# Kernel tuning notes

Measured on AMD Instinct MI355X. Metric: run time of the kernel, lower is better.

The kernel has to match this reference:

```python
import jax, jax.numpy as jnp
import numpy as np

D = 2048      # in_features == out_features == rank (forced by the module's shape algebra)
N = 8192
ALPHA = 16
SCALING = ALPHA / D
EPS = 1e-12   # F.normalize eps


def setup_inputs() -> dict:
    key = jax.random.key(0)
    kx, ka, kb, kd = jax.random.split(key, 4)
    x = jax.random.normal(kx, (N, D), dtype=jnp.float32)
    # Parameters per DoRALayer.__init__. Note: the original inits lora_B to zeros,
    # which makes the whole forward identically zero; we use small randn instead
    # so the baseline exercises non-trivial numerics (same math).
    lora_A = jax.random.normal(ka, (D, D), dtype=jnp.float32) * 0.01  # [rank, in]
    lora_B = jax.random.normal(kb, (D, D), dtype=jnp.float32) * 0.01  # [out, rank]
    magnitude = jnp.ones((D,), dtype=jnp.float32)                      # [out]
    direction = jax.random.normal(kd, (D, D), dtype=jnp.float32) * 0.01  # [out, rank]
    return {"x": x, "lora_A": lora_A, "lora_B": lora_B,
            "magnitude": magnitude, "direction": direction}


def reference(x, lora_A, lora_B, magnitude, direction):
    # W = lora_A.T @ lora_B.T  -> [in, out]
    W = jnp.einsum('ri,or->io', lora_A, lora_B)
    # F.linear(x, W) = x @ W.T  -> [N, in]
    lora_output = jnp.einsum('no,io->ni', x, W) * SCALING
    # torch.norm(magnitude): scalar L2 norm of the magnitude vector
    mag = jnp.linalg.norm(magnitude)
    # F.normalize(direction, p=2, dim=1) with eps clamp
    dnorm = jnp.sqrt(jnp.sum(direction * direction, axis=1, keepdims=True))
    dirn = direction / jnp.maximum(dnorm, EPS)
    # (direction @ lora_output.T).T  -> [N, out]
    dora_output = mag * jnp.einsum('or,nr->no', dirn, lora_output)
    return dora_output
```

## Files before the change

### kernel.cpp

```cpp
#include <hip/hip_runtime.h>

typedef unsigned short u16;
typedef unsigned int   u32;
typedef __attribute__((ext_vector_type(8))) __bf16 bf16x8;
typedef __attribute__((ext_vector_type(4))) float  f32x4;

#define D_DIM 2048
#define N_TOK 8192

__device__ __forceinline__ u16 f2bf(float f) {
  u32 u = __float_as_uint(f);
  u32 r = (u + 0x7fffu + ((u >> 16) & 1u)) >> 16;
  return (u16)r;
}

__device__ __forceinline__ void gl16(const void* g, void* l) {
  __builtin_amdgcn_global_load_lds((const __attribute__((address_space(1))) void*)g,
                                   (__attribute__((address_space(3))) void*)l,
                                   16, 0, 0);
}

__global__ __launch_bounds__(256) void cvt_f32_bf16(const float* __restrict__ in,
                                                    u16* __restrict__ out, int n4) {
  int idx = blockIdx.x * 256 + threadIdx.x;
  int stride = gridDim.x * 256;
  for (int i = idx; i < n4; i += stride) {
    float4 v = ((const float4*)in)[i];
    ushort4 o;
    o.x = f2bf(v.x); o.y = f2bf(v.y); o.z = f2bf(v.z); o.w = f2bf(v.w);
    ((ushort4*)out)[i] = o;
  }
}

__global__ __launch_bounds__(256) void normalize_rows(const float* __restrict__ dir,
                                                      u16* __restrict__ out) {
  const int row = blockIdx.x;
  const int tid = threadIdx.x;
  const float4* r = (const float4*)(dir + (size_t)row * D_DIM);
  float4 v0 = r[tid * 2 + 0];
  float4 v1 = r[tid * 2 + 1];
  float ss = v0.x*v0.x + v0.y*v0.y + v0.z*v0.z + v0.w*v0.w
           + v1.x*v1.x + v1.y*v1.y + v1.z*v1.z + v1.w*v1.w;
  #pragma unroll
  for (int off = 32; off > 0; off >>= 1) ss += __shfl_down(ss, off);
  __shared__ float red[4];
  __shared__ float invs;
  if ((tid & 63) == 0) red[tid >> 6] = ss;
  __syncthreads();
  if (tid == 0) {
    float t = red[0] + red[1] + red[2] + red[3];
    invs = 1.0f / fmaxf(sqrtf(t), 1e-12f);
  }
  __syncthreads();
  float inv = invs;
  ushort4 o0, o1;
  o0.x = f2bf(v0.x * inv); o0.y = f2bf(v0.y * inv);
  o0.z = f2bf(v0.z * inv); o0.w = f2bf(v0.w * inv);
  o1.x = f2bf(v1.x * inv); o1.y = f2bf(v1.y * inv);
  o1.z = f2bf(v1.z * inv); o1.w = f2bf(v1.w * inv);
  ushort4* ow = (ushort4*)(out + (size_t)row * D_DIM);
  ow[tid * 2 + 0] = o0;
  ow[tid * 2 + 1] = o1;
}

__global__ __launch_bounds__(256) void mag_scale_k(const float* __restrict__ m,
                                                   float* __restrict__ scale,
                                                   int n, float scaling) {
  const int tid = threadIdx.x;
  float ss = 0.0f;
  for (int i = tid; i < n / 4; i += 256) {
    float4 v = ((const float4*)m)[i];
    ss += v.x*v.x + v.y*v.y + v.z*v.z + v.w*v.w;
  }
  #pragma unroll
  for (int off = 32; off > 0; off >>= 1) ss += __shfl_down(ss, off);
  __shared__ float red[4];
  if ((tid & 63) == 0) red[tid >> 6] = ss;
  __syncthreads();
  if (tid == 0) {
    float t = red[0] + red[1] + red[2] + red[3];
    scale[0] = sqrtf(t) * scaling;
  }
}

template <int OUT_BF16>
__global__ __launch_bounds__(256)
void gemm_nt(const u16* __restrict__ A, const u16* __restrict__ B,
             void* __restrict__ Cv, int M, int Nn, int K,
             const float* __restrict__ scale_ptr) {
  __shared__ __align__(16) u16 lA[128 * 64];
  __shared__ __align__(16) u16 lB[128 * 64];
  const int tid  = threadIdx.x;
  const int lane = tid & 63;
  const int wave = tid >> 6;
  const int wr = wave >> 1, wc = wave & 1;
  const int row0 = blockIdx.y * 128, col0 = blockIdx.x * 128;

  const u16* Ag = A + (size_t)row0 * K;
  const u16* Bg = B + (size_t)col0 * K;

  f32x4 acc[4][4];
  #pragma unroll
  for (int i = 0; i < 4; ++i)
    #pragma unroll
    for (int j = 0; j < 4; ++j)
      acc[i][j] = (f32x4){0.0f, 0.0f, 0.0f, 0.0f};

  const int rsub = lane >> 3;
  const int sm   = lane & 7;

  for (int k0 = 0; k0 < K; k0 += 64) {
    #pragma unroll
    for (int j = 0; j < 4; ++j) {
      int c  = wave * 4 + j;
      int rt = c * 8 + rsub;
      int ssrc = sm ^ (rt & 7);
      gl16(Ag + (size_t)rt * K + k0 + ssrc * 8, &lA[c * 512 + lane * 8]);
      gl16(Bg + (size_t)rt * K + k0 + ssrc * 8, &lB[c * 512 + lane * 8]);
    }
    __syncthreads();

    #pragma unroll
    for (int ks = 0; ks < 2; ++ks) {
      bf16x8 af[4], bfr[4];
      #pragma unroll
      for (int mi = 0; mi < 4; ++mi) {
        int ra = wr * 64 + mi * 16 + (lane & 15);
        int sa = (ks * 4 + (lane >> 4)) ^ (ra & 7);
        af[mi] = *(const bf16x8*)&lA[ra * 64 + sa * 8];
        int rb = wc * 64 + mi * 16 + (lane & 15);
        int sb = (ks * 4 + (lane >> 4)) ^ (rb & 7);
        bfr[mi] = *(const bf16x8*)&lB[rb * 64 + sb * 8];
      }
      #pragma unroll
      for (int mi = 0; mi < 4; ++mi)
        #pragma unroll
        for (int ni = 0; ni < 4; ++ni)
          acc[mi][ni] = __builtin_amdgcn_mfma_f32_16x16x32_bf16(
              af[mi], bfr[ni], acc[mi][ni], 0, 0, 0);
    }
    __syncthreads();
  }

  float scl = scale_ptr ? scale_ptr[0] : 1.0f;
  const int orow = row0 + wr * 64 + (lane >> 4) * 4;
  const int ocol = col0 + wc * 64 + (lane & 15);
  #pragma unroll
  for (int mi = 0; mi < 4; ++mi) {
    #pragma unroll
    for (int ni = 0; ni < 4; ++ni) {
      #pragma unroll
      for (int r = 0; r < 4; ++r) {
        int gr = orow + mi * 16 + r;
        int gc = ocol + ni * 16;
        float v = acc[mi][ni][r] * scl;
        if (OUT_BF16) ((u16*)Cv)[(size_t)gr * Nn + gc] = f2bf(v);
        else          ((float*)Cv)[(size_t)gr * Nn + gc] = v;
      }
    }
  }
}

extern "C" void kernel_launch(void* const* d_in, const int* in_sizes, int n_in,
                              void* d_out, int out_size, void* d_ws, size_t ws_size,
                              hipStream_t stream) {
  const float* x    = (const float*)d_in[0];
  const float* lorA = (const float*)d_in[1];
  const float* lorB = (const float*)d_in[2];
  const float* mag  = (const float*)d_in[3];
  const float* dir  = (const float*)d_in[4];
  float* out = (float*)d_out;

  char* ws = (char*)d_ws;
  u16*   xb  = (u16*)(ws);
  u16*   Ab  = (u16*)(ws + 33554432);
  u16*   Bb  = (u16*)(ws + 41943040);
  u16*   Db  = (u16*)(ws + 50331648);
  u16*   CT  = (u16*)(ws + 58720256);
  float* scl = (float*)(ws + 67108864);
  u16*   WfT = Db;

  cvt_f32_bf16<<<2048, 256, 0, stream>>>(x,    xb, N_TOK * D_DIM / 4);
  cvt_f32_bf16<<<1024, 256, 0, stream>>>(lorA, Ab, D_DIM * D_DIM / 4);
  cvt_f32_bf16<<<1024, 256, 0, stream>>>(lorB, Bb, D_DIM * D_DIM / 4);
  normalize_rows<<<D_DIM, 256, 0, stream>>>(dir, Db);
  mag_scale_k<<<1, 256, 0, stream>>>(mag, scl, D_DIM, 16.0f / 2048.0f);

  gemm_nt<1><<<dim3(D_DIM / 128, D_DIM / 128), 256, 0, stream>>>(
      Db, Ab, CT, D_DIM, D_DIM, D_DIM, nullptr);
  gemm_nt<1><<<dim3(D_DIM / 128, D_DIM / 128), 256, 0, stream>>>(
      CT, Bb, WfT, D_DIM, D_DIM, D_DIM, nullptr);
  gemm_nt<0><<<dim3(D_DIM / 128, N_TOK / 128), 256, 0, stream>>>(
      xb, WfT, out, N_TOK, D_DIM, D_DIM, scl);
}
```

Baseline: 332.3 us.

## Use 256x256 double-buffered 8-wave GEMM for the large token projection

Result: faster. 312.9 us (-5.8%).

```diff
diff --git a/kernel.cpp b/kernel.cpp
--- a/kernel.cpp
+++ b/kernel.cpp
@@ -161,6 +161,138 @@
   }
 }
 
+#define STG(tile, half) do {                                                   \
+    const u16* G_ = ((half) < 2) ? (A + (size_t)(row0 + ((half)&1)*128) * K)   \
+                                 : (B + (size_t)(col0 + ((half)&1)*128) * K);  \
+    u16* L_ = &lds[(tile)&1][half][0];                                         \
+    const int k0_ = (tile) << 6;                                               \
+    { int idx = tid;       int rt = idx >> 3, sm2 = idx & 7;                   \
+      gl16(G_ + (size_t)rt*K + k0_ + (sm2 ^ (rt&7))*8, L_ + idx*8); }          \
+    { int idx = 512 + tid; int rt = idx >> 3, sm2 = idx & 7;                   \
+      gl16(G_ + (size_t)rt*K + k0_ + (sm2 ^ (rt&7))*8, L_ + idx*8); }          \
+  } while (0)
+
+#define RDA(b, mi, ks) (*(const bf16x8*)&lds[b][wr][((mi)*16 + fr)*64 + ((((ks)*4 + fs) ^ (fr & 7)))*8])
+#define RDB(b, ni, ks) (*(const bf16x8*)&lds[b][2 + ((wc*64 + (ni)*16 + fr) >> 7)][((wc*64 + (ni)*16 + fr) & 127)*64 + ((((ks)*4 + fs) ^ (fr & 7)))*8])
+#define MFMA(a, bb, c) __builtin_amdgcn_mfma_f32_16x16x32_bf16(a, bb, c, 0, 0, 0)
+
+template <int OUT_BF16>
+__global__ __launch_bounds__(512, 2)
+void gemm_nt8(const u16* __restrict__ A, const u16* __restrict__ B,
+              void* __restrict__ Cv, int M, int Nn, int K,
+              const float* __restrict__ scale_ptr) {
+  __shared__ __align__(16) u16 lds[2][4][128 * 64];
+  const int tid  = threadIdx.x;
+  const int lane = tid & 63;
+  const int wave = tid >> 6;
+  const int wr = wave >> 2;
+  const int wc = wave & 3;
+  const int row0 = blockIdx.y * 256, col0 = blockIdx.x * 256;
+  const int NT = K >> 6;
+  const int fr = lane & 15, fs = lane >> 4;
+
+  f32x4 acc[8][4];
+  #pragma unroll
+  for (int i = 0; i < 8; ++i)
+    #pragma unroll
+    for (int j = 0; j < 4; ++j)
+      acc[i][j] = (f32x4){0.0f, 0.0f, 0.0f, 0.0f};
+
+  STG(0, 0); STG(0, 1); STG(0, 2); STG(0, 3);
+  if (NT > 1) {
+    STG(1, 0); STG(1, 1); STG(1, 2); STG(1, 3);
+    asm volatile("s_waitcnt vmcnt(8)" ::: "memory");
+  } else {
+    asm volatile("s_waitcnt vmcnt(0)" ::: "memory");
+  }
+  __builtin_amdgcn_s_barrier();
+
+  for (int t = 0; t < NT; ++t) {
+    const int b = t & 1;
+    bf16x8 aF[8], bL[4], bH[4];
+
+    #pragma unroll
+    for (int mi = 0; mi < 4; ++mi) { aF[mi*2] = RDA(b, mi, 0); aF[mi*2+1] = RDA(b, mi, 1); }
+    #pragma unroll
+    for (int ni = 0; ni < 2; ++ni) { bL[ni*2] = RDB(b, ni, 0); bL[ni*2+1] = RDB(b, ni, 1); }
+    __builtin_amdgcn_s_barrier();
+    asm volatile("s_waitcnt lgkmcnt(0)");
+    __builtin_amdgcn_s_setprio(1);
+    #pragma unroll
+    for (int mi = 0; mi < 4; ++mi)
+      #pragma unroll
+      for (int ni = 0; ni < 2; ++ni)
+        #pragma unroll
+        for (int ks = 0; ks < 2; ++ks)
+          acc[mi][ni] = MFMA(aF[mi*2+ks], bL[ni*2+ks], acc[mi][ni]);
+    __builtin_amdgcn_s_setprio(0);
+    __builtin_amdgcn_s_barrier();
+
+    #pragma unroll
+    for (int ni = 0; ni < 2; ++ni) { bH[ni*2] = RDB(b, ni + 2, 0); bH[ni*2+1] = RDB(b, ni + 2, 1); }
+    __builtin_amdgcn_s_barrier();
+    asm volatile("s_waitcnt lgkmcnt(0)");
+    __builtin_amdgcn_s_setprio(1);
+    #pragma unroll
+    for (int mi = 0; mi < 4; ++mi)
+      #pragma unroll
+      for (int ni = 0; ni < 2; ++ni)
+        #pragma unroll
+        for (int ks = 0; ks < 2; ++ks)
+          acc[mi][ni + 2] = MFMA(aF[mi*2+ks], bH[ni*2+ks], acc[mi][ni + 2]);
+    __builtin_amdgcn_s_setprio(0);
+    __builtin_amdgcn_s_barrier();
+
+    #pragma unroll
+    for (int mi = 0; mi < 4; ++mi) { aF[mi*2] = RDA(b, mi + 4, 0); aF[mi*2+1] = RDA(b, mi + 4, 1); }
+    if (t + 2 < NT) { STG(t + 2, 2); STG(t + 2, 3); }
+    __builtin_amdgcn_s_barrier();
+    asm volatile("s_waitcnt lgkmcnt(0)");
+    __builtin_amdgcn_s_setprio(1);
+    #pragma unroll
+    for (int mi = 0; mi < 4; ++mi)
+      #pragma unroll
+      for (int ni = 0; ni < 2; ++ni)
+        #pragma unroll
+        for (int ks = 0; ks < 2; ++ks)
+          acc[mi + 4][ni + 2] = MFMA(aF[mi*2+ks], bH[ni*2+ks], acc[mi + 4][ni + 2]);
+    __builtin_amdgcn_s_setprio(0);
+    __builtin_amdgcn_s_barrier();
+
+    if (t + 2 < NT) { STG(t + 2, 0); STG(t + 2, 1); }
+    __builtin_amdgcn_s_barrier();
+    asm volatile("s_waitcnt lgkmcnt(0)");
+    __builtin_amdgcn_s_setprio(1);
+    #pragma unroll
+    for (int mi = 0; mi < 4; ++mi)
+      #pragma unroll
+      for (int ni = 0; ni < 2; ++ni)
+        #pragma unroll
+        for (int ks = 0; ks < 2; ++ks)
+          acc[mi + 4][ni] = MFMA(aF[mi*2+ks], bL[ni*2+ks], acc[mi + 4][ni]);
+    __builtin_amdgcn_s_setprio(0);
+    if (t < NT - 2) asm volatile("s_waitcnt vmcnt(8)" ::: "memory");
+    else            asm volatile("s_waitcnt vmcnt(0)" ::: "memory");
+    __builtin_amdgcn_s_barrier();
+  }
+
+  float scl = scale_ptr ? scale_ptr[0] : 1.0f;
+  #pragma unroll
+  for (int mi = 0; mi < 8; ++mi) {
+    #pragma unroll
+    for (int ni = 0; ni < 4; ++ni) {
+      #pragma unroll
+      for (int r = 0; r < 4; ++r) {
+        int gr = row0 + wr * 128 + mi * 16 + fs * 4 + r;
+        int gc = col0 + wc * 64 + ni * 16 + fr;
+        float v = acc[mi][ni][r] * scl;
+        if (OUT_BF16) ((u16*)Cv)[(size_t)gr * Nn + gc] = f2bf(v);
+        else          ((float*)Cv)[(size_t)gr * Nn + gc] = v;
+      }
+    }
+  }
+}
+
 extern "C" void kernel_launch(void* const* d_in, const int* in_sizes, int n_in,
                               void* d_out, int out_size, void* d_ws, size_t ws_size,
                               hipStream_t stream) {
@@ -190,6 +322,6 @@
       Db, Ab, CT, D_DIM, D_DIM, D_DIM, nullptr);
   gemm_nt<1><<<dim3(D_DIM / 128, D_DIM / 128), 256, 0, stream>>>(
       CT, Bb, WfT, D_DIM, D_DIM, D_DIM, nullptr);
-  gemm_nt<0><<<dim3(D_DIM / 128, N_TOK / 128), 256, 0, stream>>>(
+  gemm_nt8<0><<<dim3(D_DIM / 256, N_TOK / 256), 512, 0, stream>>>(
       xb, WfT, out, N_TOK, D_DIM, D_DIM, scl);
 }
```
